# Optimization experiments

Measured on AMD Instinct MI355X. Metric: run time of the kernel, lower is better.

## Reference

```python
import jax, jax.numpy as jnp
import numpy as np

N_HEADS = 16
D_EMBD = 1024
D_HEAD = D_EMBD // N_HEADS  # 64


def setup_inputs() -> dict:
    key = jax.random.key(0)
    k0, k1, k2, k3, k4 = jax.random.split(key, 5)
    s = 1.0 / np.sqrt(D_EMBD)
    return {
        "x": jax.random.normal(k0, (4, 2048, D_EMBD), dtype=jnp.float32),
        "w_in": jax.random.normal(k1, (D_EMBD, 3 * D_EMBD), dtype=jnp.float32) * s,
        "b_in": jax.random.normal(k2, (3 * D_EMBD,), dtype=jnp.float32) * 0.02,
        "w_out": jax.random.normal(k3, (D_EMBD, D_EMBD), dtype=jnp.float32) * s,
        "b_out": jax.random.normal(k4, (D_EMBD,), dtype=jnp.float32) * 0.02,
    }


def reference(x, w_in, b_in, w_out, b_out):
    B, S, D = x.shape
    # fused QKV projection; torch .chunk(3) order in source is k, q, v
    kqv = x @ w_in + b_in                      # [B, S, 3D]
    k, q, v = jnp.split(kqv, 3, axis=-1)
    # split heads: [B, S, D] -> [B, H, S, Dh]
    def heads(t):
        return t.reshape(B, S, N_HEADS, D_HEAD).transpose(0, 2, 1, 3)
    q, k, v = heads(q), heads(k), heads(v)
    # attention scores, explicit O(S^2) matrix (naive, unmasked path)
    scores = jnp.einsum("bhsd,bhtd->bhst", q, k) / jnp.sqrt(
        jnp.asarray(D_HEAD, dtype=x.dtype)
    )
    probs = jax.nn.softmax(scores, axis=-1)    # [B, H, S, S]
    out = jnp.einsum("bhst,bhtd->bhsd", probs, v)
    out = out.transpose(0, 2, 1, 3).reshape(B, S, D)
    return out @ w_out + b_out
```

## Files before the change

### kernel.cpp

```cpp
#include <hip/hip_runtime.h>

typedef unsigned short u16;
typedef __attribute__((ext_vector_type(8))) short bf16x8;
typedef __attribute__((ext_vector_type(4))) float f32x4;

#define MFMA(a, b, c) __builtin_amdgcn_mfma_f32_16x16x32_bf16(a, b, c, 0, 0, 0)

#if defined(__has_builtin)
#if __has_builtin(__builtin_amdgcn_exp2f)
#define EXP2(x) __builtin_amdgcn_exp2f(x)
#endif
#endif
#ifndef EXP2
#define EXP2(x) exp2f(x)
#endif

#define ASYNC16(g, l)                                                      \
  __builtin_amdgcn_global_load_lds(                                        \
      (const __attribute__((address_space(1))) void*)(g),                  \
      (__attribute__((address_space(3))) void*)(l), 16, 0, 0)

#define MEMFENCE() asm volatile("" ::: "memory")

__device__ __forceinline__ u16 f2bf(float x) {
  union { float f; unsigned u; } v; v.f = x;
  unsigned r = (v.u + 0x7fffu + ((v.u >> 16) & 1u)) >> 16;
  return (u16)r;
}

__device__ __forceinline__ unsigned pack_bf2(float a, float b) {
  unsigned ua = __float_as_uint(a) + 0x8000u;
  unsigned ub = __float_as_uint(b) + 0x8000u;
  return __builtin_amdgcn_perm(ub, ua, 0x07060302u);
}

__global__ void transpose_to_bf16(const float* __restrict__ in, u16* __restrict__ out,
                                  int R, int C) {
  __shared__ float tile[32][33];
  int c0 = blockIdx.x * 32, r0 = blockIdx.y * 32;
  int tx = threadIdx.x, ty = threadIdx.y;
#pragma unroll
  for (int i = 0; i < 32; i += 8)
    tile[ty + i][tx] = in[(size_t)(r0 + ty + i) * C + c0 + tx];
  __syncthreads();
#pragma unroll
  for (int i = 0; i < 32; i += 8)
    out[(size_t)(c0 + ty + i) * R + r0 + tx] = f2bf(tile[tx][ty + i]);
}

__global__ void f32_to_bf16_vec(const float4* __restrict__ in, uint2* __restrict__ out) {
  int idx = blockIdx.x * 256 + threadIdx.x;
  float4 v = in[idx];
  out[idx] = make_uint2(pack_bf2(v.x, v.y), pack_bf2(v.z, v.w));
}

#define BM 128
#define BN 128
#define BK 64

template <int OUT_F32>
__global__ __launch_bounds__(256, 2) void gemm_bt(const u16* __restrict__ A,
                                                  const u16* __restrict__ Bt,
                                                  const float* __restrict__ bias,
                                                  void* __restrict__ Cout,
                                                  int M, int N, int K, int ldc,
                                                  int sc_lo, int sc_hi, float qs) {
  __shared__ __align__(16) u16 As[BM * BK];
  __shared__ __align__(16) u16 Bs[BN * BK];
  int bn = blockIdx.x * BN, bm = blockIdx.y * BM;
  int tid = threadIdx.x;
  int wave = tid >> 6, lane = tid & 63;
  int quad = lane >> 4, l16 = lane & 15;
  int wm = (wave >> 1) * 64, wn = (wave & 1) * 64;

  f32x4 acc[4][4] = {};

  int lrow = lane >> 3, lcol = (lane & 7) * 8;
  const u16* gA = A + (size_t)(bm + wave * 8 + lrow) * K + lcol;
  const u16* gB = Bt + (size_t)(bn + wave * 8 + lrow) * K + lcol;
  u16* lA = &As[wave * 8 * BK];
  u16* lB = &Bs[wave * 8 * BK];

  for (int k0 = 0; k0 < K; k0 += BK) {
#pragma unroll
    for (int p = 0; p < 4; ++p) {
      ASYNC16(gA + (size_t)p * 32 * K, lA + p * 32 * BK);
      ASYNC16(gB + (size_t)p * 32 * K, lB + p * 32 * BK);
    }
    gA += BK;
    gB += BK;
    __syncthreads();
#pragma unroll
    for (int kk = 0; kk < BK; kk += 32) {
      bf16x8 af[4], bfr[4];
#pragma unroll
      for (int i = 0; i < 4; ++i)
        af[i] = *(const bf16x8*)&As[(wm + 16 * i + l16) * BK + kk + quad * 8];
#pragma unroll
      for (int j = 0; j < 4; ++j)
        bfr[j] = *(const bf16x8*)&Bs[(wn + 16 * j + l16) * BK + kk + quad * 8];
#pragma unroll
      for (int i = 0; i < 4; ++i)
#pragma unroll
        for (int j = 0; j < 4; ++j)
          acc[i][j] = MFMA(af[i], bfr[j], acc[i][j]);
    }
    __syncthreads();
  }

#pragma unroll
  for (int i = 0; i < 4; ++i) {
#pragma unroll
    for (int j = 0; j < 4; ++j) {
      int gn = bn + wn + 16 * j + l16;
      float bv = bias[gn];
      float sc = (gn >= sc_lo && gn < sc_hi) ? qs : 1.0f;
#pragma unroll
      for (int r = 0; r < 4; ++r) {
        int gm = bm + wm + 16 * i + quad * 4 + r;
        float v = (acc[i][j][r] + bv) * sc;
        if (OUT_F32)
          ((float*)Cout)[(size_t)gm * ldc + gn] = v;
        else
          ((u16*)Cout)[(size_t)gm * ldc + gn] = f2bf(v);
      }
    }
  }
}

#define SEQ 2048
#define ROWS3 3072

__global__ void v_transpose(const u16* __restrict__ kqv, u16* __restrict__ vt) {
  int bh = blockIdx.y;
  int b = bh >> 4, h = bh & 15;
  int t0 = blockIdx.x * 64;
  int tid = threadIdx.x;
  __shared__ u16 tile[64][72];
  int r = tid >> 3, c = (tid & 7) * 8;
#pragma unroll
  for (int p = 0; p < 2; ++p)
    *(uint4*)&tile[p * 32 + r][c] =
        *(const uint4*)&kqv[(size_t)b * SEQ * ROWS3 + (size_t)(t0 + p * 32 + r) * ROWS3 +
                            2048 + h * 64 + c];
  __syncthreads();
#pragma unroll
  for (int p = 0; p < 2; ++p) {
    int d = p * 32 + r;
    u16 tmp[8];
#pragma unroll
    for (int i = 0; i < 8; ++i) {
      int pos = c + i;
      int k = 16 * (pos & 3) + (pos >> 2);
      tmp[i] = tile[k][d];
    }
    *(uint4*)&vt[(size_t)bh * 64 * SEQ + (size_t)d * SEQ + t0 + c] = *(uint4*)tmp;
  }
}

__global__ __launch_bounds__(256, 4) void attn_kernel(const u16* __restrict__ kqv,
                                                      const u16* __restrict__ vt,
                                                      u16* __restrict__ out) {
  int g = blockIdx.x;
  int bh = g & 63, qtile = g >> 6;
  int b = bh >> 4, h = bh & 15;
  int tid = threadIdx.x, wave = tid >> 6, lane = tid & 63;
  int quad = lane >> 4, l16 = lane & 15;

  __shared__ __align__(16) u16 Ks[2][64 * 64];
  __shared__ __align__(16) u16 Vts[2][64 * 64];
  __shared__ __align__(16) u16 Ps[4][16 * 64];

  const u16* base = kqv + (size_t)b * SEQ * ROWS3;
  int hcol = h * 64;
  const u16* vbase = vt + (size_t)bh * 64 * SEQ;

  bf16x8 qf[2][2];
#pragma unroll
  for (int t = 0; t < 2; ++t) {
    int s = qtile * 128 + wave * 32 + t * 16 + l16;
    const u16* qrow = base + (size_t)s * ROWS3 + 1024 + hcol;
    qf[t][0] = *(const bf16x8*)(qrow + quad * 8);
    qf[t][1] = *(const bf16x8*)(qrow + 32 + quad * 8);
  }

  bf16x8 ones;
#pragma unroll
  for (int i = 0; i < 8; ++i) ones[i] = (short)0x3F80;

  f32x4 o[2][4] = {};
  f32x4 ol[2] = {};
  const f32x4 zf = {};
  u16* pw = &Ps[wave][0];

  int prow = lane & 7;
  int pchk = (lane >> 3) * 8;

  int rb2 = (l16 >> 3) * 512;
  int r8 = (l16 & 7) * 8;

  int pm8 = (l16 & 7) * 8;
  int prd0 = l16 * 64 + ((quad * 8) ^ pm8);
  int prd1 = l16 * 64 + ((32 + quad * 8) ^ pm8);
  int pwr[4];
#pragma unroll
  for (int r = 0; r < 4; ++r) {
    int rho = quad * 4 + r;
    pwr[r] = rho * 64 + ((4 * l16) ^ ((rho & 7) * 8));
  }

  const u16* kg = base + hcol + (size_t)(wave * 16 + prow) * ROWS3 + pchk;
  const u16* vg = vbase + (size_t)(wave * 16 + prow) * SEQ + pchk;

  ASYNC16(kg, &Ks[0][wave * 16 * 64]);
  ASYNC16(kg + (size_t)8 * ROWS3, &Ks[0][(wave * 16 + 8) * 64]);
  ASYNC16(vg, &Vts[0][wave * 16 * 64]);
  ASYNC16(vg + (size_t)8 * SEQ, &Vts[0][(wave * 16 + 8) * 64]);

  int cur = 0;

  for (int t0 = 0; t0 < SEQ; t0 += 64) {
    __syncthreads();

    if (t0 + 64 < SEQ) {
      kg += (size_t)64 * ROWS3;
      vg += 64;
      ASYNC16(kg, &Ks[cur ^ 1][wave * 16 * 64]);
      ASYNC16(kg + (size_t)8 * ROWS3, &Ks[cur ^ 1][(wave * 16 + 8) * 64]);
      ASYNC16(vg, &Vts[cur ^ 1][wave * 16 * 64]);
      ASYNC16(vg + (size_t)8 * SEQ, &Vts[cur ^ 1][(wave * 16 + 8) * 64]);
    }

    const u16* ks = &Ks[cur][0];
    const u16* vs = &Vts[cur][0];

    f32x4 s0[4], s1[4];
#pragma unroll
    for (int j = 0; j < 4; ++j) {
      bf16x8 k0 = *(const bf16x8*)&ks[j * 1024 + rb2 + quad * 64 + r8];
      bf16x8 k1 = *(const bf16x8*)&ks[j * 1024 + rb2 + 256 + quad * 64 + r8];
      s0[j] = MFMA(qf[0][0], k0, zf);
      s0[j] = MFMA(qf[0][1], k1, s0[j]);
      s1[j] = MFMA(qf[1][0], k0, zf);
      s1[j] = MFMA(qf[1][1], k1, s1[j]);
    }

    bf16x8 pa[2][2];
#pragma unroll
    for (int r = 0; r < 4; ++r) {
      uint2 pk;
      pk.x = pack_bf2(EXP2(s0[0][r]), EXP2(s0[1][r]));
      pk.y = pack_bf2(EXP2(s0[2][r]), EXP2(s0[3][r]));
      *(uint2*)&pw[pwr[r]] = pk;
    }
    MEMFENCE();
    pa[0][0] = *(const bf16x8*)&pw[prd0];
    pa[0][1] = *(const bf16x8*)&pw[prd1];
    MEMFENCE();
#pragma unroll
    for (int r = 0; r < 4; ++r) {
      uint2 pk;
      pk.x = pack_bf2(EXP2(s1[0][r]), EXP2(s1[1][r]));
      pk.y = pack_bf2(EXP2(s1[2][r]), EXP2(s1[3][r]));
      *(uint2*)&pw[pwr[r]] = pk;
    }
    MEMFENCE();
    pa[1][0] = *(const bf16x8*)&pw[prd0];
    pa[1][1] = *(const bf16x8*)&pw[prd1];

#pragma unroll
    for (int d = 0; d < 4; ++d) {
      bf16x8 v0 = *(const bf16x8*)&vs[d * 1024 + rb2 + quad * 64 + r8];
      bf16x8 v1 = *(const bf16x8*)&vs[d * 1024 + rb2 + 256 + quad * 64 + r8];
      o[0][d] = MFMA(pa[0][0], v0, o[0][d]);
      o[0][d] = MFMA(pa[0][1], v1, o[0][d]);
      o[1][d] = MFMA(pa[1][0], v0, o[1][d]);
      o[1][d] = MFMA(pa[1][1], v1, o[1][d]);
    }
    ol[0] = MFMA(pa[0][0], ones, ol[0]);
    ol[0] = MFMA(pa[0][1], ones, ol[0]);
    ol[1] = MFMA(pa[1][0], ones, ol[1]);
    ol[1] = MFMA(pa[1][1], ones, ol[1]);

    cur ^= 1;
  }

#pragma unroll
  for (int t = 0; t < 2; ++t)
#pragma unroll
    for (int r = 0; r < 4; ++r) {
      float inv = 1.0f / ol[t][r];
      int s = qtile * 128 + wave * 32 + t * 16 + quad * 4 + r;
      u16* orow = out + (size_t)(b * SEQ + s) * 1024 + hcol;
#pragma unroll
      for (int d = 0; d < 4; ++d) orow[16 * d + l16] = f2bf(o[t][d][r] * inv);
    }
}

extern "C" void kernel_launch(void* const* d_in, const int* in_sizes, int n_in,
                              void* d_out, int out_size, void* d_ws, size_t ws_size,
                              hipStream_t stream) {
  const float* x     = (const float*)d_in[0];
  const float* w_in  = (const float*)d_in[1];
  const float* b_in  = (const float*)d_in[2];
  const float* w_out = (const float*)d_in[3];
  const float* b_out = (const float*)d_in[4];
  float* outp = (float*)d_out;

  char* p = (char*)d_ws;
  u16* wT_in  = (u16*)p; p += (size_t)3072 * 1024 * 2;
  u16* wT_out = (u16*)p; p += (size_t)1024 * 1024 * 2;
  u16* xb     = (u16*)p; p += (size_t)8192 * 1024 * 2;
  u16* kqv    = (u16*)p; p += (size_t)8192 * 3072 * 2;
  u16* attn   = (u16*)p;
  u16* vtbuf  = xb;

  transpose_to_bf16<<<dim3(3072 / 32, 1024 / 32), dim3(32, 8), 0, stream>>>(w_in, wT_in, 1024, 3072);
  transpose_to_bf16<<<dim3(1024 / 32, 1024 / 32), dim3(32, 8), 0, stream>>>(w_out, wT_out, 1024, 1024);
  f32_to_bf16_vec<<<dim3(8192), dim3(256), 0, stream>>>((const float4*)x, (uint2*)xb);

  const float QSCALE = 0.125f * 1.44269504088896f;
  gemm_bt<0><<<dim3(3072 / BN, 8192 / BM), 256, 0, stream>>>(
      xb, wT_in, b_in, (void*)kqv, 8192, 3072, 1024, 3072, 1024, 2048, QSCALE);

  v_transpose<<<dim3(SEQ / 64, 64), 256, 0, stream>>>(kqv, vtbuf);

  attn_kernel<<<dim3(1024), 256, 0, stream>>>(kqv, vtbuf, attn);

  gemm_bt<1><<<dim3(1024 / BN, 8192 / BM), 256, 0, stream>>>(
      attn, wT_out, b_out, (void*)outp, 8192, 1024, 1024, 1024, 0, 0, 1.0f);
}
```

Before: 278.3 us.

## Keep attention probabilities in registers via transposed S MFMA and XCD-swizzled GEMM grid

The attention kernel now computes S transposed by swapping the MFMA operands, so the exp'd scores already sit in the register layout the PV MFMA expects. This removes the per-wave LDS round trip for P, and the V transpose permutation is changed to match the new key ordering. The GEMM launches become a 1D grid with a swizzle that maps consecutive block IDs to the same XCD for better L2 locality. s_setprio is also raised around the MFMA section. The risks are correctness depending on the V permutation matching the new layout, and the swizzle assumes a grid size divisible by 8.

```diff
diff --git a/kernel.cpp b/kernel.cpp
--- a/kernel.cpp
+++ b/kernel.cpp
@@ -20,8 +20,6 @@
       (const __attribute__((address_space(1))) void*)(g),                  \
       (__attribute__((address_space(3))) void*)(l), 16, 0, 0)
 
-#define MEMFENCE() asm volatile("" ::: "memory")
-
 __device__ __forceinline__ u16 f2bf(float x) {
   union { float f; unsigned u; } v; v.f = x;
   unsigned r = (v.u + 0x7fffu + ((v.u >> 16) & 1u)) >> 16;
@@ -32,6 +30,15 @@
   unsigned ua = __float_as_uint(a) + 0x8000u;
   unsigned ub = __float_as_uint(b) + 0x8000u;
   return __builtin_amdgcn_perm(ub, ua, 0x07060302u);
+}
+
+__device__ __forceinline__ bf16x8 exp_pack8(const f32x4 a, const f32x4 b) {
+  union { unsigned u[4]; bf16x8 v; } r;
+  r.u[0] = pack_bf2(EXP2(a[0]), EXP2(a[1]));
+  r.u[1] = pack_bf2(EXP2(a[2]), EXP2(a[3]));
+  r.u[2] = pack_bf2(EXP2(b[0]), EXP2(b[1]));
+  r.u[3] = pack_bf2(EXP2(b[2]), EXP2(b[3]));
+  return r.v;
 }
 
 __global__ void transpose_to_bf16(const float* __restrict__ in, u16* __restrict__ out,
@@ -58,7 +65,7 @@
 #define BN 128
 #define BK 64
 
-template <int OUT_F32>
+template <int OUT_F32, int NBX>
 __global__ __launch_bounds__(256, 2) void gemm_bt(const u16* __restrict__ A,
                                                   const u16* __restrict__ Bt,
                                                   const float* __restrict__ bias,
@@ -67,7 +74,10 @@
                                                   int sc_lo, int sc_hi, float qs) {
   __shared__ __align__(16) u16 As[BM * BK];
   __shared__ __align__(16) u16 Bs[BN * BK];
-  int bn = blockIdx.x * BN, bm = blockIdx.y * BM;
+  int id = blockIdx.x;
+  int cpx = gridDim.x >> 3;
+  int swz = (id & 7) * cpx + (id >> 3);
+  int bn = (swz % NBX) * BN, bm = (swz / NBX) * BM;
   int tid = threadIdx.x;
   int wave = tid >> 6, lane = tid & 63;
   int quad = lane >> 4, l16 = lane & 15;
@@ -151,7 +161,7 @@
 #pragma unroll
     for (int i = 0; i < 8; ++i) {
       int pos = c + i;
-      int k = 16 * (pos & 3) + (pos >> 2);
+      int k = 16 * (2 * (pos >> 5) + ((pos >> 2) & 1)) + ((pos >> 3) & 3) * 4 + (pos & 3);
       tmp[i] = tile[k][d];
     }
     *(uint4*)&vt[(size_t)bh * 64 * SEQ + (size_t)d * SEQ + t0 + c] = *(uint4*)tmp;
@@ -169,7 +179,6 @@
 
   __shared__ __align__(16) u16 Ks[2][64 * 64];
   __shared__ __align__(16) u16 Vts[2][64 * 64];
-  __shared__ __align__(16) u16 Ps[4][16 * 64];
 
   const u16* base = kqv + (size_t)b * SEQ * ROWS3;
   int hcol = h * 64;
@@ -191,23 +200,12 @@
   f32x4 o[2][4] = {};
   f32x4 ol[2] = {};
   const f32x4 zf = {};
-  u16* pw = &Ps[wave][0];
 
   int prow = lane & 7;
   int pchk = (lane >> 3) * 8;
 
   int rb2 = (l16 >> 3) * 512;
   int r8 = (l16 & 7) * 8;
-
-  int pm8 = (l16 & 7) * 8;
-  int prd0 = l16 * 64 + ((quad * 8) ^ pm8);
-  int prd1 = l16 * 64 + ((32 + quad * 8) ^ pm8);
-  int pwr[4];
-#pragma unroll
-  for (int r = 0; r < 4; ++r) {
-    int rho = quad * 4 + r;
-    pwr[r] = rho * 64 + ((4 * l16) ^ ((rho & 7) * 8));
-  }
 
   const u16* kg = base + hcol + (size_t)(wave * 16 + prow) * ROWS3 + pchk;
   const u16* vg = vbase + (size_t)(wave * 16 + prow) * SEQ + pchk;
@@ -234,39 +232,24 @@
     const u16* ks = &Ks[cur][0];
     const u16* vs = &Vts[cur][0];
 
+    __builtin_amdgcn_s_setprio(1);
+
     f32x4 s0[4], s1[4];
 #pragma unroll
     for (int j = 0; j < 4; ++j) {
       bf16x8 k0 = *(const bf16x8*)&ks[j * 1024 + rb2 + quad * 64 + r8];
       bf16x8 k1 = *(const bf16x8*)&ks[j * 1024 + rb2 + 256 + quad * 64 + r8];
-      s0[j] = MFMA(qf[0][0], k0, zf);
-      s0[j] = MFMA(qf[0][1], k1, s0[j]);
-      s1[j] = MFMA(qf[1][0], k0, zf);
-      s1[j] = MFMA(qf[1][1], k1, s1[j]);
+      s0[j] = MFMA(k0, qf[0][0], zf);
+      s0[j] = MFMA(k1, qf[0][1], s0[j]);
+      s1[j] = MFMA(k0, qf[1][0], zf);
+      s1[j] = MFMA(k1, qf[1][1], s1[j]);
     }
 
     bf16x8 pa[2][2];
-#pragma unroll
-    for (int r = 0; r < 4; ++r) {
-      uint2 pk;
-      pk.x = pack_bf2(EXP2(s0[0][r]), EXP2(s0[1][r]));
-      pk.y = pack_bf2(EXP2(s0[2][r]), EXP2(s0[3][r]));
-      *(uint2*)&pw[pwr[r]] = pk;
-    }
-    MEMFENCE();
-    pa[0][0] = *(const bf16x8*)&pw[prd0];
-    pa[0][1] = *(const bf16x8*)&pw[prd1];
-    MEMFENCE();
-#pragma unroll
-    for (int r = 0; r < 4; ++r) {
-      uint2 pk;
-      pk.x = pack_bf2(EXP2(s1[0][r]), EXP2(s1[1][r]));
-      pk.y = pack_bf2(EXP2(s1[2][r]), EXP2(s1[3][r]));
-      *(uint2*)&pw[pwr[r]] = pk;
-    }
-    MEMFENCE();
-    pa[1][0] = *(const bf16x8*)&pw[prd0];
-    pa[1][1] = *(const bf16x8*)&pw[prd1];
+    pa[0][0] = exp_pack8(s0[0], s0[1]);
+    pa[0][1] = exp_pack8(s0[2], s0[3]);
+    pa[1][0] = exp_pack8(s1[0], s1[1]);
+    pa[1][1] = exp_pack8(s1[2], s1[3]);
 
 #pragma unroll
     for (int d = 0; d < 4; ++d) {
@@ -281,6 +264,8 @@
     ol[0] = MFMA(pa[0][1], ones, ol[0]);
     ol[1] = MFMA(pa[1][0], ones, ol[1]);
     ol[1] = MFMA(pa[1][1], ones, ol[1]);
+
+    __builtin_amdgcn_s_setprio(0);
 
     cur ^= 1;
   }
@@ -320,13 +305,13 @@
   f32_to_bf16_vec<<<dim3(8192), dim3(256), 0, stream>>>((const float4*)x, (uint2*)xb);
 
   const float QSCALE = 0.125f * 1.44269504088896f;
-  gemm_bt<0><<<dim3(3072 / BN, 8192 / BM), 256, 0, stream>>>(
+  gemm_bt<0, 3072 / BN><<<dim3((3072 / BN) * (8192 / BM)), 256, 0, stream>>>(
       xb, wT_in, b_in, (void*)kqv, 8192, 3072, 1024, 3072, 1024, 2048, QSCALE);
 
   v_transpose<<<dim3(SEQ / 64, 64), 256, 0, stream>>>(kqv, vtbuf);
 
   attn_kernel<<<dim3(1024), 256, 0, stream>>>(kqv, vtbuf, attn);
 
-  gemm_bt<1><<<dim3(1024 / BN, 8192 / BM), 256, 0, stream>>>(
+  gemm_bt<1, 1024 / BN><<<dim3((1024 / BN) * (8192 / BM)), 256, 0, stream>>>(
       attn, wT_out, b_out, (void*)outp, 8192, 1024, 1024, 1024, 0, 0, 1.0f);
 }
```

After: 279.3 us. No clear change (+0.4%).
